# Performance work log

Hardware: AMD Instinct MI355X
Metric: run time of the kernel (lower is better)

## Reference

```python
import jax, jax.numpy as jnp
import numpy as np

N = 262144  # number of points
W = 256     # feature width


def setup_inputs() -> dict:
    key = jax.random.key(0)
    k1, k2, k3 = jax.random.split(key, 3)
    x = jax.random.normal(k1, (N, W), dtype=jnp.float32)
    # torch nn.Linear(W, 9) layout: weight [out, in], bias [out]
    fc_w = jax.random.normal(k2, (9, W), dtype=jnp.float32) * (1.0 / np.sqrt(W))
    fc_b = jax.random.normal(k3, (9,), dtype=jnp.float32) * 0.01
    return {"x": x, "fc_w": fc_w, "fc_b": fc_b}


def symmetric_orthogonalization(m):
    # m: [n, 3, 3] -> nearest rotation matrix (special orthogonal Procrustes)
    u, s, vt = jnp.linalg.svd(m, full_matrices=False)
    det = jnp.linalg.det(jnp.einsum('nij,njk->nik', u, vt))  # [n]
    ones = jnp.ones_like(det)
    d = jnp.stack([ones, ones, det], axis=-1)  # [n, 3] diag(1, 1, det)
    r = jnp.einsum('nij,nj,njk->nik', u, d, vt)
    return r


def reference(x, fc_w, fc_b):
    # x: [N, W] -> rotations flattened to [N, 9] (out_type='mat', out_rots=1)
    y = x @ fc_w.T + fc_b            # [N, 9]
    m = y.reshape(-1, 3, 3)          # [N, 3, 3]
    r = symmetric_orthogonalization(m)
    return r.reshape(x.shape[:-1] + (9,))
```

## Files before the change

kernel.cpp:

```cpp
#include <hip/hip_runtime.h>
#include <math.h>

#define N_PTS 262144
#define WIDTH 256

__device__ __forceinline__ void jrot(double &app, double &aqq, double &apq,
                                     double &arp, double &arq,
                                     double &vp0, double &vq0,
                                     double &vp1, double &vq1,
                                     double &vp2, double &vq2)
{
    double a = apq;
    if (fabs(a) < 1e-300) return;
    double theta = (aqq - app) / (2.0 * a);
    double tt = copysign(1.0, theta) / (fabs(theta) + sqrt(1.0 + theta * theta));
    double c = 1.0 / sqrt(1.0 + tt * tt);
    double s = tt * c;
    app -= tt * a;
    aqq += tt * a;
    apq = 0.0;
    double rp = arp, rq = arq;
    arp = c * rp - s * rq;
    arq = s * rp + c * rq;
    double t0p = vp0, t0q = vq0; vp0 = c * t0p - s * t0q; vq0 = s * t0p + c * t0q;
    double t1p = vp1, t1q = vq1; vp1 = c * t1p - s * t1q; vq1 = s * t1p + c * t1q;
    double t2p = vp2, t2q = vq2; vp2 = c * t2p - s * t2q; vq2 = s * t2p + c * t2q;
}

__global__ __launch_bounds__(256) void so3_kernel(
    const float* __restrict__ x,
    const float* __restrict__ fw,
    const float* __restrict__ fb,
    float* __restrict__ out)
{
    __shared__ float xs[256][33];
    const int t  = threadIdx.x;
    const int p0 = blockIdx.x << 8;

    float y[9];
#pragma unroll
    for (int j = 0; j < 9; ++j) y[j] = 0.f;

    for (int kc = 0; kc < 8; ++kc) {
        const int k0 = kc << 5;
#pragma unroll
        for (int i = 0; i < 8; ++i) {
            const int flat = (i << 8) + t;
            const int row  = flat >> 3;
            const int c4   = flat & 7;
            const float4 v = *reinterpret_cast<const float4*>(
                x + (size_t)(p0 + row) * WIDTH + k0 + (c4 << 2));
            xs[row][(c4 << 2) + 0] = v.x;
            xs[row][(c4 << 2) + 1] = v.y;
            xs[row][(c4 << 2) + 2] = v.z;
            xs[row][(c4 << 2) + 3] = v.w;
        }
        __syncthreads();
#pragma unroll
        for (int kk = 0; kk < 32; ++kk) {
            const float xv = xs[t][kk];
            const int k = k0 + kk;
#pragma unroll
            for (int j = 0; j < 9; ++j)
                y[j] = fmaf(xv, fw[j * WIDTH + k], y[j]);
        }
        __syncthreads();
    }
#pragma unroll
    for (int j = 0; j < 9; ++j) y[j] += fb[j];

    const double m00 = y[0], m01 = y[1], m02 = y[2];
    const double m10 = y[3], m11 = y[4], m12 = y[5];
    const double m20 = y[6], m21 = y[7], m22 = y[8];

    double a00 = m00*m00 + m10*m10 + m20*m20;
    double a01 = m00*m01 + m10*m11 + m20*m21;
    double a02 = m00*m02 + m10*m12 + m20*m22;
    double a11 = m01*m01 + m11*m11 + m21*m21;
    double a12 = m01*m02 + m11*m12 + m21*m22;
    double a22 = m02*m02 + m12*m12 + m22*m22;

    double v[3][3] = { {1,0,0}, {0,1,0}, {0,0,1} };

#pragma unroll
    for (int sw = 0; sw < 4; ++sw) {
        jrot(a00, a11, a01, a02, a12,
             v[0][0], v[0][1], v[1][0], v[1][1], v[2][0], v[2][1]);
        jrot(a00, a22, a02, a01, a12,
             v[0][0], v[0][2], v[1][0], v[1][2], v[2][0], v[2][2]);
        jrot(a11, a22, a12, a01, a02,
             v[0][1], v[0][2], v[1][1], v[1][2], v[2][1], v[2][2]);
    }

    double d0 = a00, d1 = a11, d2 = a22, tmp;
    if (d0 < d1) { tmp=d0; d0=d1; d1=tmp;
        tmp=v[0][0]; v[0][0]=v[0][1]; v[0][1]=tmp;
        tmp=v[1][0]; v[1][0]=v[1][1]; v[1][1]=tmp;
        tmp=v[2][0]; v[2][0]=v[2][1]; v[2][1]=tmp; }
    if (d0 < d2) { tmp=d0; d0=d2; d2=tmp;
        tmp=v[0][0]; v[0][0]=v[0][2]; v[0][2]=tmp;
        tmp=v[1][0]; v[1][0]=v[1][2]; v[1][2]=tmp;
        tmp=v[2][0]; v[2][0]=v[2][2]; v[2][2]=tmp; }
    if (d1 < d2) { tmp=d1; d1=d2; d2=tmp;
        tmp=v[0][1]; v[0][1]=v[0][2]; v[0][2]=tmp;
        tmp=v[1][1]; v[1][1]=v[1][2]; v[1][2]=tmp;
        tmp=v[2][1]; v[2][1]=v[2][2]; v[2][2]=tmp; }

    const double v1x = v[0][0], v1y = v[1][0], v1z = v[2][0];
    const double v2x = v[0][1], v2y = v[1][1], v2z = v[2][1];

    double u1x = m00*v1x + m01*v1y + m02*v1z;
    double u1y = m10*v1x + m11*v1y + m12*v1z;
    double u1z = m20*v1x + m21*v1y + m22*v1z;
    double inv1 = 1.0 / (sqrt(u1x*u1x + u1y*u1y + u1z*u1z) + 1e-300);
    u1x *= inv1; u1y *= inv1; u1z *= inv1;

    double u2x = m00*v2x + m01*v2y + m02*v2z;
    double u2y = m10*v2x + m11*v2y + m12*v2z;
    double u2z = m20*v2x + m21*v2y + m22*v2z;
    const double d12 = u1x*u2x + u1y*u2y + u1z*u2z;
    u2x -= d12*u1x; u2y -= d12*u1y; u2z -= d12*u1z;
    double inv2 = 1.0 / (sqrt(u2x*u2x + u2y*u2y + u2z*u2z) + 1e-300);
    u2x *= inv2; u2y *= inv2; u2z *= inv2;

    const double u3x = u1y*u2z - u1z*u2y;
    const double u3y = u1z*u2x - u1x*u2z;
    const double u3z = u1x*u2y - u1y*u2x;
    const double v3x = v1y*v2z - v1z*v2y;
    const double v3y = v1z*v2x - v1x*v2z;
    const double v3z = v1x*v2y - v1y*v2x;

    float r[9];
    r[0] = (float)(u1x*v1x + u2x*v2x + u3x*v3x);
    r[1] = (float)(u1x*v1y + u2x*v2y + u3x*v3y);
    r[2] = (float)(u1x*v1z + u2x*v2z + u3x*v3z);
    r[3] = (float)(u1y*v1x + u2y*v2x + u3y*v3x);
    r[4] = (float)(u1y*v1y + u2y*v2y + u3y*v3y);
    r[5] = (float)(u1y*v1z + u2y*v2z + u3y*v3z);
    r[6] = (float)(u1z*v1x + u2z*v2x + u3z*v3x);
    r[7] = (float)(u1z*v1y + u2z*v2y + u3z*v3y);
    r[8] = (float)(u1z*v1z + u2z*v2z + u3z*v3z);

    float* o = out + (size_t)(p0 + t) * 9;
#pragma unroll
    for (int j = 0; j < 9; ++j) o[j] = r[j];
}

extern "C" void kernel_launch(void* const* d_in, const int* in_sizes, int n_in,
                              void* d_out, int out_size, void* d_ws, size_t ws_size,
                              hipStream_t stream) {
    const float* x  = (const float*)d_in[0];
    const float* fw = (const float*)d_in[1];
    const float* fb = (const float*)d_in[2];
    float* out = (float*)d_out;
    dim3 grid(N_PTS / 256), block(256);
    hipLaunchKernelGGL(so3_kernel, grid, block, 0, stream, x, fw, fb, out);
}
```

Measured before the change: 74.45 us.

## Switch SVD math to fp32 and register-prefetch x tiles

Converts the Jacobi eigen-solve and rotation reconstruction from double to float precision, adding one extra sweep to make up for reduced accuracy. Restructures the x loading into 16-wide chunks with register prefetch of the next chunk overlapping the FMA loop, and sets a launch-bounds occupancy hint. The aim is to remove slow fp64 ALU work and hide global load latency. The cost is lower numerical accuracy for ill-conditioned matrices and more barriers per block.

After: 69.53 us. 6.6% less time.

```diff
diff --git a/kernel.cpp b/kernel.cpp
--- a/kernel.cpp
+++ b/kernel.cpp
@@ -4,36 +4,36 @@
 #define N_PTS 262144
 #define WIDTH 256
 
-__device__ __forceinline__ void jrot(double &app, double &aqq, double &apq,
-                                     double &arp, double &arq,
-                                     double &vp0, double &vq0,
-                                     double &vp1, double &vq1,
-                                     double &vp2, double &vq2)
+__device__ __forceinline__ void jrot(float &app, float &aqq, float &apq,
+                                     float &arp, float &arq,
+                                     float &vp0, float &vq0,
+                                     float &vp1, float &vq1,
+                                     float &vp2, float &vq2)
 {
-    double a = apq;
-    if (fabs(a) < 1e-300) return;
-    double theta = (aqq - app) / (2.0 * a);
-    double tt = copysign(1.0, theta) / (fabs(theta) + sqrt(1.0 + theta * theta));
-    double c = 1.0 / sqrt(1.0 + tt * tt);
-    double s = tt * c;
+    float a = apq;
+    if (fabsf(a) < 1e-20f) return;
+    float theta = (aqq - app) / (2.0f * a);
+    float tt = copysignf(1.0f, theta) / (fabsf(theta) + sqrtf(1.0f + theta * theta));
+    float c = 1.0f / sqrtf(1.0f + tt * tt);
+    float s = tt * c;
     app -= tt * a;
     aqq += tt * a;
-    apq = 0.0;
-    double rp = arp, rq = arq;
+    apq = 0.0f;
+    float rp = arp, rq = arq;
     arp = c * rp - s * rq;
     arq = s * rp + c * rq;
-    double t0p = vp0, t0q = vq0; vp0 = c * t0p - s * t0q; vq0 = s * t0p + c * t0q;
-    double t1p = vp1, t1q = vq1; vp1 = c * t1p - s * t1q; vq1 = s * t1p + c * t1q;
-    double t2p = vp2, t2q = vq2; vp2 = c * t2p - s * t2q; vq2 = s * t2p + c * t2q;
+    float t0p = vp0, t0q = vq0; vp0 = c * t0p - s * t0q; vq0 = s * t0p + c * t0q;
+    float t1p = vp1, t1q = vq1; vp1 = c * t1p - s * t1q; vq1 = s * t1p + c * t1q;
+    float t2p = vp2, t2q = vq2; vp2 = c * t2p - s * t2q; vq2 = s * t2p + c * t2q;
 }
 
-__global__ __launch_bounds__(256) void so3_kernel(
+__global__ __launch_bounds__(256, 4) void so3_kernel(
     const float* __restrict__ x,
     const float* __restrict__ fw,
     const float* __restrict__ fb,
     float* __restrict__ out)
 {
-    __shared__ float xs[256][33];
+    __shared__ float xs[256][17];
     const int t  = threadIdx.x;
     const int p0 = blockIdx.x << 8;
 
@@ -41,23 +41,44 @@
 #pragma unroll
     for (int j = 0; j < 9; ++j) y[j] = 0.f;
 
-    for (int kc = 0; kc < 8; ++kc) {
-        const int k0 = kc << 5;
+    float4 pre[4];
 #pragma unroll
-        for (int i = 0; i < 8; ++i) {
+    for (int i = 0; i < 4; ++i) {
+        const int flat = (i << 8) + t;
+        const int row  = flat >> 2;
+        const int c4   = flat & 3;
+        pre[i] = *reinterpret_cast<const float4*>(
+            x + (size_t)(p0 + row) * WIDTH + (c4 << 2));
+    }
+
+    for (int kc = 0; kc < 16; ++kc) {
+#pragma unroll
+        for (int i = 0; i < 4; ++i) {
             const int flat = (i << 8) + t;
-            const int row  = flat >> 3;
-            const int c4   = flat & 7;
-            const float4 v = *reinterpret_cast<const float4*>(
-                x + (size_t)(p0 + row) * WIDTH + k0 + (c4 << 2));
-            xs[row][(c4 << 2) + 0] = v.x;
-            xs[row][(c4 << 2) + 1] = v.y;
-            xs[row][(c4 << 2) + 2] = v.z;
-            xs[row][(c4 << 2) + 3] = v.w;
+            const int row  = flat >> 2;
+            const int c    = (flat & 3) << 2;
+            xs[row][c + 0] = pre[i].x;
+            xs[row][c + 1] = pre[i].y;
+            xs[row][c + 2] = pre[i].z;
+            xs[row][c + 3] = pre[i].w;
         }
         __syncthreads();
+
+        if (kc < 15) {
+            const int k0n = (kc + 1) << 4;
 #pragma unroll
-        for (int kk = 0; kk < 32; ++kk) {
+            for (int i = 0; i < 4; ++i) {
+                const int flat = (i << 8) + t;
+                const int row  = flat >> 2;
+                const int c4   = flat & 3;
+                pre[i] = *reinterpret_cast<const float4*>(
+                    x + (size_t)(p0 + row) * WIDTH + k0n + (c4 << 2));
+            }
+        }
+
+        const int k0 = kc << 4;
+#pragma unroll
+        for (int kk = 0; kk < 16; ++kk) {
             const float xv = xs[t][kk];
             const int k = k0 + kk;
 #pragma unroll
@@ -66,24 +87,25 @@
         }
         __syncthreads();
     }
+
 #pragma unroll
     for (int j = 0; j < 9; ++j) y[j] += fb[j];
 
-    const double m00 = y[0], m01 = y[1], m02 = y[2];
-    const double m10 = y[3], m11 = y[4], m12 = y[5];
-    const double m20 = y[6], m21 = y[7], m22 = y[8];
+    const float m00 = y[0], m01 = y[1], m02 = y[2];
+    const float m10 = y[3], m11 = y[4], m12 = y[5];
+    const float m20 = y[6], m21 = y[7], m22 = y[8];
 
-    double a00 = m00*m00 + m10*m10 + m20*m20;
-    double a01 = m00*m01 + m10*m11 + m20*m21;
-    double a02 = m00*m02 + m10*m12 + m20*m22;
-    double a11 = m01*m01 + m11*m11 + m21*m21;
-    double a12 = m01*m02 + m11*m12 + m21*m22;
-    double a22 = m02*m02 + m12*m12 + m22*m22;
+    float a00 = m00*m00 + m10*m10 + m20*m20;
+    float a01 = m00*m01 + m10*m11 + m20*m21;
+    float a02 = m00*m02 + m10*m12 + m20*m22;
+    float a11 = m01*m01 + m11*m11 + m21*m21;
+    float a12 = m01*m02 + m11*m12 + m21*m22;
+    float a22 = m02*m02 + m12*m12 + m22*m22;
 
-    double v[3][3] = { {1,0,0}, {0,1,0}, {0,0,1} };
+    float v[3][3] = { {1,0,0}, {0,1,0}, {0,0,1} };
 
 #pragma unroll
-    for (int sw = 0; sw < 4; ++sw) {
+    for (int sw = 0; sw < 5; ++sw) {
         jrot(a00, a11, a01, a02, a12,
              v[0][0], v[0][1], v[1][0], v[1][1], v[2][0], v[2][1]);
         jrot(a00, a22, a02, a01, a12,
@@ -92,7 +114,7 @@
              v[0][1], v[0][2], v[1][1], v[1][2], v[2][1], v[2][2]);
     }
 
-    double d0 = a00, d1 = a11, d2 = a22, tmp;
+    float d0 = a00, d1 = a11, d2 = a22, tmp;
     if (d0 < d1) { tmp=d0; d0=d1; d1=tmp;
         tmp=v[0][0]; v[0][0]=v[0][1]; v[0][1]=tmp;
         tmp=v[1][0]; v[1][0]=v[1][1]; v[1][1]=tmp;
@@ -106,40 +128,40 @@
         tmp=v[1][1]; v[1][1]=v[1][2]; v[1][2]=tmp;
         tmp=v[2][1]; v[2][1]=v[2][2]; v[2][2]=tmp; }
 
-    const double v1x = v[0][0], v1y = v[1][0], v1z = v[2][0];
-    const double v2x = v[0][1], v2y = v[1][1], v2z = v[2][1];
+    const float v1x = v[0][0], v1y = v[1][0], v1z = v[2][0];
+    const float v2x = v[0][1], v2y = v[1][1], v2z = v[2][1];
 
-    double u1x = m00*v1x + m01*v1y + m02*v1z;
-    double u1y = m10*v1x + m11*v1y + m12*v1z;
-    double u1z = m20*v1x + m21*v1y + m22*v1z;
-    double inv1 = 1.0 / (sqrt(u1x*u1x + u1y*u1y + u1z*u1z) + 1e-300);
+    float u1x = m00*v1x + m01*v1y + m02*v1z;
+    float u1y = m10*v1x + m11*v1y + m12*v1z;
+    float u1z = m20*v1x + m21*v1y + m22*v1z;
+    float inv1 = 1.0f / (sqrtf(u1x*u1x + u1y*u1y + u1z*u1z) + 1e-30f);
     u1x *= inv1; u1y *= inv1; u1z *= inv1;
 
-    double u2x = m00*v2x + m01*v2y + m02*v2z;
-    double u2y = m10*v2x + m11*v2y + m12*v2z;
-    double u2z = m20*v2x + m21*v2y + m22*v2z;
-    const double d12 = u1x*u2x + u1y*u2y + u1z*u2z;
+    float u2x = m00*v2x + m01*v2y + m02*v2z;
+    float u2y = m10*v2x + m11*v2y + m12*v2z;
+    float u2z = m20*v2x + m21*v2y + m22*v2z;
+    const float d12 = u1x*u2x + u1y*u2y + u1z*u2z;
     u2x -= d12*u1x; u2y -= d12*u1y; u2z -= d12*u1z;
-    double inv2 = 1.0 / (sqrt(u2x*u2x + u2y*u2y + u2z*u2z) + 1e-300);
+    float inv2 = 1.0f / (sqrtf(u2x*u2x + u2y*u2y + u2z*u2z) + 1e-30f);
     u2x *= inv2; u2y *= inv2; u2z *= inv2;
 
-    const double u3x = u1y*u2z - u1z*u2y;
-    const double u3y = u1z*u2x - u1x*u2z;
-    const double u3z = u1x*u2y - u1y*u2x;
-    const double v3x = v1y*v2z - v1z*v2y;
-    const double v3y = v1z*v2x - v1x*v2z;
-    const double v3z = v1x*v2y - v1y*v2x;
+    const float u3x = u1y*u2z - u1z*u2y;
+    const float u3y = u1z*u2x - u1x*u2z;
+    const float u3z = u1x*u2y - u1y*u2x;
+    const float v3x = v1y*v2z - v1z*v2y;
+    const float v3y = v1z*v2x - v1x*v2z;
+    const float v3z = v1x*v2y - v1y*v2x;
 
     float r[9];
-    r[0] = (float)(u1x*v1x + u2x*v2x + u3x*v3x);
-    r[1] = (float)(u1x*v1y + u2x*v2y + u3x*v3y);
-    r[2] = (float)(u1x*v1z + u2x*v2z + u3x*v3z);
-    r[3] = (float)(u1y*v1x + u2y*v2x + u3y*v3x);
-    r[4] = (float)(u1y*v1y + u2y*v2y + u3y*v3y);
-    r[5] = (float)(u1y*v1z + u2y*v2z + u3y*v3z);
-    r[6] = (float)(u1z*v1x + u2z*v2x + u3z*v3x);
-    r[7] = (float)(u1z*v1y + u2z*v2y + u3z*v3y);
-    r[8] = (float)(u1z*v1z + u2z*v2z + u3z*v3z);
+    r[0] = u1x*v1x + u2x*v2x + u3x*v3x;
+    r[1] = u1x*v1y + u2x*v2y + u3x*v3y;
+    r[2] = u1x*v1z + u2x*v2z + u3x*v3z;
+    r[3] = u1y*v1x + u2y*v2x + u3y*v3x;
+    r[4] = u1y*v1y + u2y*v2y + u3y*v3y;
+    r[5] = u1y*v1z + u2y*v2z + u3y*v3z;
+    r[6] = u1z*v1x + u2z*v2x + u3z*v3x;
+    r[7] = u1z*v1y + u2z*v2y + u3z*v3y;
+    r[8] = u1z*v1z + u2z*v2z + u3z*v3z;
 
     float* o = out + (size_t)(p0 + t) * 9;
 #pragma unroll
```
